# Kernel tuning notes

Hardware: AMD Instinct MI355X
Metric: run time of the kernel (lower is better)

The kernel has to match this reference:

```python
import jax, jax.numpy as jnp
import numpy as np

N = 262144   # tokens
L = 128      # ldims (per-direction LSTM feature size)
H = 128      # hidden_units
H2 = 128     # hidden2_units
R = 64       # number of relation labels


def setup_inputs() -> dict:
    key = jax.random.key(0)
    ks = jax.random.split(key, 12)
    glorot = lambda k, shape: jax.random.uniform(
        k, shape, jnp.float32, -1.0, 1.0) * np.sqrt(6.0 / (shape[0] + shape[1]))
    return {
        "fwd": jax.random.normal(ks[0], (N, L), jnp.float32),
        "bwd": jax.random.normal(ks[1], (N, L), jnp.float32),
        "gold_heads": jax.random.randint(ks[2], (N - 1,), 0, N),
        "gold_rels": jax.random.randint(ks[3], (N - 1,), 0, R),
        "WFOH": glorot(ks[4], (2 * L, H)),
        "WFOM": glorot(ks[5], (2 * L, H)),
        "rhidBias": glorot(ks[6], (1, H)),
        "rcatBias": glorot(ks[7], (1, 2 * H)),
        "rhid2Layer": glorot(ks[8], (2 * H, H2)),
        "rhid2Bias": glorot(ks[9], (1, H2)),
        "routLayer": glorot(ks[10], (H2, R)),
        "routBias": glorot(ks[11], (1, R)),
    }


def reference(fwd, bwd, gold_heads, gold_rels, WFOH, WFOM, rhidBias,
              rcatBias, rhid2Layer, rhid2Bias, routLayer, routBias):
    E = gold_heads.shape[0]
    mods = jnp.arange(E) + 1                       # modifiers are tokens 1..N-1
    # per-edge concat(head fwd-state, modifier bwd-state): (E, 2L)
    cat = jnp.concatenate([fwd[gold_heads], bwd[mods]], axis=-1)
    headfov = cat @ WFOH                           # (E, H)
    modfov = cat @ WFOM                            # (E, H)
    # hidden2_units > 0 branch of __evaluateLabel
    h = jnp.tanh(jnp.concatenate([headfov, modfov], axis=-1) + rcatBias)  # (E, 2H)
    h2 = jnp.tanh(h @ rhid2Layer + rhid2Bias)      # (E, H2)
    scores = h2 @ routLayer + routBias             # (E, R)
    # hinge: best wrong label vs gold label, loss only if margin violated
    gold_s = jnp.take_along_axis(scores, gold_rels[:, None], axis=1)[:, 0]
    masked = jnp.where(jnp.arange(R)[None, :] == gold_rels[:, None], -jnp.inf, scores)
    wrong_idx = jnp.argmax(masked, axis=1)
    wrong_s = jnp.take_along_axis(scores, wrong_idx[:, None], axis=1)[:, 0]
    lerrs = jnp.where(gold_s < wrong_s + 1.0, wrong_s - gold_s, 0.0)  # (E,)
    return lerrs
```

## Files before the change

kernel.cpp:

```cpp
#include <hip/hip_runtime.h>
#include <hip/hip_bf16.h>

typedef __bf16 bf16x8 __attribute__((ext_vector_type(8)));
typedef __bf16 bf16x2 __attribute__((ext_vector_type(2)));
typedef float  f32x4  __attribute__((ext_vector_type(4)));

#define MFMA16 __builtin_amdgcn_mfma_f32_16x16x32_bf16

__device__ __forceinline__ float fast_tanh(float x) {
    float e = __builtin_amdgcn_exp2f(x * 2.8853900817779268f);
    return 1.0f - 2.0f * __builtin_amdgcn_rcpf(e + 1.0f);
}

__device__ __forceinline__ int kinv(int ke) {
    return (ke & ~31) | ((ke & 1) << 4) | ((ke >> 1) & 15);
}

__global__ __launch_bounds__(256) void preconv_kernel(
    const float* __restrict__ WFOH, const float* __restrict__ WFOM,
    const float* __restrict__ rhid2Layer, const float* __restrict__ routLayer,
    char* __restrict__ ws)
{
    const int f = blockIdx.x * 256 + threadIdx.x;
    bf16x8 v;
    char* dst;
    if (f < 8192) {
        const int lane = f & 63, t = f >> 6;
        const int nbl = t & 1, kk = (t >> 1) & 7, w = t >> 4;
        const int g = lane >> 4, c = lane & 15;
        const int nb = 32 * w + 16 * nbl;
        const float* Wsrc = (nb < 128) ? WFOH : WFOM;
        const int col = (nb + c) & 127;
        #pragma unroll
        for (int j = 0; j < 8; ++j) v[j] = (__bf16)Wsrc[(32 * kk + 8 * g + j) * 128 + col];
        dst = ws + (size_t)f * 16;
    } else if (f < 12288) {
        const int f2 = f - 8192;
        const int lane = f2 & 63, t = f2 >> 6;
        const int nbl = t & 1, kk = (t >> 1) & 7, q4 = t >> 4;
        const int g = lane >> 4, c = lane & 15;
        const int n2 = 32 * q4 + 16 * nbl + c;
        #pragma unroll
        for (int j = 0; j < 8; ++j) v[j] = (__bf16)rhid2Layer[kinv(32 * kk + 8 * g + j) * 128 + n2];
        dst = ws + 131072 + (size_t)f2 * 16;
    } else if (f < 13312) {
        const int f3 = f - 12288;
        const int lane = f3 & 63, t = f3 >> 6;
        const int kk = t & 3, q4 = t >> 2;
        const int g = lane >> 4, c = lane & 15;
        const int n3 = 16 * q4 + c;
        #pragma unroll
        for (int j = 0; j < 8; ++j) v[j] = (__bf16)routLayer[kinv(32 * kk + 8 * g + j) * 64 + n3];
        dst = ws + 196608 + (size_t)f3 * 16;
    } else {
        return;
    }
    *(bf16x8*)dst = v;
}

template<bool PRE>
__device__ __forceinline__ bf16x8 wfrag1(const char* ws, const float* WFOH, const float* WFOM,
                                         int w, int kk, int nbl, int lane) {
    if constexpr (PRE) {
        return *(const bf16x8*)(ws + (size_t)w * 16384 + kk * 2048 + nbl * 1024 + lane * 16);
    } else {
        const int g = lane >> 4, c = lane & 15;
        const int nb = 32 * w + 16 * nbl;
        const float* Wsrc = (nb < 128) ? WFOH : WFOM;
        const int col = (nb + c) & 127;
        bf16x8 v;
        #pragma unroll
        for (int j = 0; j < 8; ++j) v[j] = (__bf16)Wsrc[(32 * kk + 8 * g + j) * 128 + col];
        return v;
    }
}
template<bool PRE>
__device__ __forceinline__ bf16x8 wfrag2(const char* ws, const float* rhid2Layer,
                                         int q4, int kk, int nbl, int lane) {
    if constexpr (PRE) {
        return *(const bf16x8*)(ws + 131072 + (size_t)q4 * 16384 + kk * 2048 + nbl * 1024 + lane * 16);
    } else {
        const int g = lane >> 4, c = lane & 15;
        const int n2 = 32 * q4 + 16 * nbl + c;
        bf16x8 v;
        #pragma unroll
        for (int j = 0; j < 8; ++j) v[j] = (__bf16)rhid2Layer[kinv(32 * kk + 8 * g + j) * 128 + n2];
        return v;
    }
}
template<bool PRE>
__device__ __forceinline__ bf16x8 wfrag3(const char* ws, const float* routLayer,
                                         int q4, int kk, int lane) {
    if constexpr (PRE) {
        return *(const bf16x8*)(ws + 196608 + (size_t)q4 * 4096 + kk * 1024 + lane * 16);
    } else {
        const int g = lane >> 4, c = lane & 15;
        const int n3 = 16 * q4 + c;
        bf16x8 v;
        #pragma unroll
        for (int j = 0; j < 8; ++j) v[j] = (__bf16)routLayer[kinv(32 * kk + 8 * g + j) * 64 + n3];
        return v;
    }
}

template<bool PRE>
__global__ __launch_bounds__(512, 2) void rel_kernel(
    const float* __restrict__ fwd, const float* __restrict__ bwd,
    const int* __restrict__ gold_heads, const int* __restrict__ gold_rels,
    const float* __restrict__ WFOH, const float* __restrict__ WFOM,
    const float* __restrict__ rcatBias, const float* __restrict__ rhid2Layer,
    const float* __restrict__ rhid2Bias, const float* __restrict__ routLayer,
    const float* __restrict__ routBias, const char* __restrict__ ws,
    float* __restrict__ out, int E, int NT)
{
    __shared__ __align__(16) char smem[131072];
    __shared__ int sh_nfix;
    __shared__ int sh_fixlist[16];

    char* const sh_cat = smem;
    char* const sh_h   = smem + 65536;
    float* const fx_cat = (float*)(smem + 98304);
    float* const fx_h   = fx_cat + 256;
    float* const fx_h2  = fx_h + 256;
    float* const fx_p   = fx_h2 + 128;

    const int tid   = threadIdx.x;
    const int w     = tid >> 6;
    const int lane  = tid & 63;
    const int row16 = lane & 15;
    const int g     = lane >> 4;
    const int xm    = (row16 & 7) << 4;
    const int q4    = w & 3;
    const int hw    = w >> 2;

    const int r_s = tid >> 2;
    const int q_s = tid & 3;
    const int xr  = (r_s & 7) << 4;

    const float rcb0 = rcatBias[32 * w + row16];
    const float rcb1 = rcatBias[32 * w + 16 + row16];
    const float r2b0 = rhid2Bias[32 * q4 + row16];
    const float r2b1 = rhid2Bias[32 * q4 + 16 + row16];
    const float rob  = routBias[16 * q4 + row16];

    bf16x8 pfb[8];
    {
        const int e = blockIdx.x * 128 + r_s;
        int nh = 0;
        if (q_s < 2 && e < E) nh = gold_heads[e];
        if (e < E) {
            const float* src = (q_s < 2) ? (fwd + (size_t)nh * 128 + 64 * q_s)
                                         : (bwd + (size_t)(e + 1) * 128 + 64 * (q_s - 2));
            const float4* p4 = (const float4*)src;
            #pragma unroll
            for (int i = 0; i < 8; ++i) {
                const float4 a = p4[2 * i], b = p4[2 * i + 1];
                bf16x8 t;
                t[0] = (__bf16)a.x; t[1] = (__bf16)a.y; t[2] = (__bf16)a.z; t[3] = (__bf16)a.w;
                t[4] = (__bf16)b.x; t[5] = (__bf16)b.y; t[6] = (__bf16)b.z; t[7] = (__bf16)b.w;
                pfb[i] = t;
            }
        } else {
            #pragma unroll
            for (int i = 0; i < 8; ++i) {
                bf16x8 t;
                #pragma unroll
                for (int j = 0; j < 8; ++j) t[j] = (__bf16)0.0f;
                pfb[i] = t;
            }
        }
    }

    for (int tile = blockIdx.x; tile < NT; tile += gridDim.x) {
        const int e0 = tile * 128;
        const int tnext = tile + gridDim.x;
        const bool hn = tnext < NT;

        #pragma unroll
        for (int i = 0; i < 8; ++i)
            *(bf16x8*)(sh_cat + r_s * 512 + ((128 * q_s + 16 * i) ^ xr)) = pfb[i];

        int nh = 0;
        bool gv = false;
        if (hn) {
            const int en = tnext * 128 + r_s;
            gv = en < E;
            if (q_s < 2 && gv) nh = gold_heads[en];
        }
        __syncthreads();

        f32x4 acc1[8][2];
        #pragma unroll
        for (int i = 0; i < 8; ++i) {
            acc1[i][0] = (f32x4){0.f, 0.f, 0.f, 0.f};
            acc1[i][1] = (f32x4){0.f, 0.f, 0.f, 0.f};
        }
        #pragma unroll 1
        for (int kk = 0; kk < 8; ++kk) {
            const bf16x8 b0 = wfrag1<PRE>(ws, WFOH, WFOM, w, kk, 0, lane);
            const bf16x8 b1 = wfrag1<PRE>(ws, WFOH, WFOM, w, kk, 1, lane);
            const int ko = (64 * kk + 16 * g) ^ xm;
            #pragma unroll
            for (int mb = 0; mb < 8; ++mb) {
                const bf16x8 a = *(const bf16x8*)(sh_cat + (16 * mb + row16) * 512 + ko);
                acc1[mb][0] = MFMA16(a, b0, acc1[mb][0], 0, 0, 0);
                acc1[mb][1] = MFMA16(a, b1, acc1[mb][1], 0, 0, 0);
            }
        }
        #pragma unroll
        for (int mb = 0; mb < 8; ++mb) {
            #pragma unroll
            for (int r = 0; r < 4; ++r) {
                const int row = 16 * mb + 4 * g + r;
                bf16x2 p;
                p[0] = (__bf16)fast_tanh(acc1[mb][0][r] + rcb0);
                p[1] = (__bf16)fast_tanh(acc1[mb][1][r] + rcb1);
                *(bf16x2*)(sh_h + row * 512 + ((64 * w + 4 * row16) ^ ((row & 7) << 4))) = p;
            }
        }
        __syncthreads();

        const float* gsrc = nullptr;
        if (hn) {
            const int en = tnext * 128 + r_s;
            gsrc = (q_s < 2) ? (fwd + (size_t)nh * 128 + 64 * q_s)
                             : (bwd + (size_t)(en + 1) * 128 + 64 * (q_s - 2));
        }
        float4 pfA[8];
        if (hn && gv) {
            const float4* p4 = (const float4*)gsrc;
            #pragma unroll
            for (int i = 0; i < 8; ++i) pfA[i] = p4[i];
        } else {
            #pragma unroll
            for (int i = 0; i < 8; ++i) pfA[i] = make_float4(0.f, 0.f, 0.f, 0.f);
        }

        f32x4 acc2[4][2];
        #pragma unroll
        for (int i = 0; i < 4; ++i) {
            acc2[i][0] = (f32x4){0.f, 0.f, 0.f, 0.f};
            acc2[i][1] = (f32x4){0.f, 0.f, 0.f, 0.f};
        }
        #pragma unroll 1
        for (int kk = 0; kk < 8; ++kk) {
            const bf16x8 b0 = wfrag2<PRE>(ws, rhid2Layer, q4, kk, 0, lane);
            const bf16x8 b1 = wfrag2<PRE>(ws, rhid2Layer, q4, kk, 1, lane);
            const int ko = (64 * kk + 16 * g) ^ xm;
            #pragma unroll
            for (int i = 0; i < 4; ++i) {
                const bf16x8 a = *(const bf16x8*)(sh_h + (16 * (4 * hw + i) + row16) * 512 + ko);
                acc2[i][0] = MFMA16(a, b0, acc2[i][0], 0, 0, 0);
                acc2[i][1] = MFMA16(a, b1, acc2[i][1], 0, 0, 0);
            }
        }
        #pragma unroll
        for (int i = 0; i < 4; ++i) {
            const float4 a = pfA[2 * i], b = pfA[2 * i + 1];
            bf16x8 t;
            t[0] = (__bf16)a.x; t[1] = (__bf16)a.y; t[2] = (__bf16)a.z; t[3] = (__bf16)a.w;
            t[4] = (__bf16)b.x; t[5] = (__bf16)b.y; t[6] = (__bf16)b.z; t[7] = (__bf16)b.w;
            pfb[i] = t;
        }
        float4 pfB[8];
        if (hn && gv) {
            const float4* p4 = (const float4*)gsrc;
            #pragma unroll
            for (int i = 0; i < 8; ++i) pfB[i] = p4[8 + i];
        } else {
            #pragma unroll
            for (int i = 0; i < 8; ++i) pfB[i] = make_float4(0.f, 0.f, 0.f, 0.f);
        }
        #pragma unroll
        for (int i = 0; i < 4; ++i) {
            #pragma unroll
            for (int r = 0; r < 4; ++r) {
                const int row = 16 * (4 * hw + i) + 4 * g + r;
                bf16x2 p;
                p[0] = (__bf16)fast_tanh(acc2[i][0][r] + r2b0);
                p[1] = (__bf16)fast_tanh(acc2[i][1][r] + r2b1);
                *(bf16x2*)(sh_cat + row * 256 + ((64 * q4 + 4 * row16) ^ ((row & 7) << 4))) = p;
            }
        }
        __syncthreads();

        if (tid == 0) sh_nfix = 0;
        f32x4 acc3[4];
        #pragma unroll
        for (int i = 0; i < 4; ++i) acc3[i] = (f32x4){0.f, 0.f, 0.f, 0.f};
        #pragma unroll
        for (int kk = 0; kk < 4; ++kk) {
            const bf16x8 b = wfrag3<PRE>(ws, routLayer, q4, kk, lane);
            const int ko = (64 * kk + 16 * g) ^ xm;
            #pragma unroll
            for (int i = 0; i < 4; ++i) {
                const bf16x8 a = *(const bf16x8*)(sh_cat + (16 * (4 * hw + i) + row16) * 256 + ko);
                acc3[i] = MFMA16(a, b, acc3[i], 0, 0, 0);
            }
        }
        #pragma unroll
        for (int i = 0; i < 4; ++i) {
            const float4 a = pfB[2 * i], b = pfB[2 * i + 1];
            bf16x8 t;
            t[0] = (__bf16)a.x; t[1] = (__bf16)a.y; t[2] = (__bf16)a.z; t[3] = (__bf16)a.w;
            t[4] = (__bf16)b.x; t[5] = (__bf16)b.y; t[6] = (__bf16)b.z; t[7] = (__bf16)b.w;
            pfb[4 + i] = t;
        }
        #pragma unroll
        for (int i = 0; i < 4; ++i) {
            #pragma unroll
            for (int r = 0; r < 4; ++r) {
                const int row = 16 * (4 * hw + i) + 4 * g + r;
                *(float*)(sh_h + row * 256 + ((64 * q4 + 4 * row16) ^ ((row & 7) << 4))) = acc3[i][r] + rob;
            }
        }
        __syncthreads();

        {
            const int r = tid >> 2, q = tid & 3;
            const int e = e0 + r;
            const int gold = (e < E) ? gold_rels[e] : 0;
            float gs = -3.0e38f, ws_ = -3.0e38f;
            #pragma unroll
            for (int c = 0; c < 4; ++c) {
                const f32x4 sv = *(const f32x4*)(sh_h + r * 256 + ((64 * q + 16 * c) ^ ((r & 7) << 4)));
                #pragma unroll
                for (int cc = 0; cc < 4; ++cc) {
                    const int lab = 16 * q + 4 * c + cc;
                    const float v = sv[cc];
                    if (lab == gold) gs = v; else ws_ = fmaxf(ws_, v);
                }
            }
            gs = fmaxf(gs, __shfl_xor(gs, 1)); ws_ = fmaxf(ws_, __shfl_xor(ws_, 1));
            gs = fmaxf(gs, __shfl_xor(gs, 2)); ws_ = fmaxf(ws_, __shfl_xor(ws_, 2));
            if (q == 0 && e < E) {
                out[e] = (gs < ws_ + 1.0f) ? (ws_ - gs) : 0.0f;
                if (fabsf((gs - ws_) - 1.0f) < 0.125f) {
                    const int idx = atomicAdd(&sh_nfix, 1);
                    if (idx < 16) sh_fixlist[idx] = r;
                }
            }
        }
        __syncthreads();

        int nf = sh_nfix; if (nf > 16) nf = 16;
        for (int fi = 0; fi < nf; ++fi) {
            const int e = e0 + sh_fixlist[fi];
            if (tid < 256) {
                const int head = gold_heads[e];
                fx_cat[tid] = (tid < 128) ? fwd[(size_t)head * 128 + tid]
                                          : bwd[(size_t)(e + 1) * 128 + (tid - 128)];
            }
            __syncthreads();
            {
                const int d = tid & 255, half = tid >> 8;
                const float* base = (d < 128) ? WFOH : WFOM;
                const int col = d & 127;
                float s = 0.f;
                #pragma unroll 8
                for (int k = 128 * half; k < 128 * half + 128; ++k) s += fx_cat[k] * base[k * 128 + col];
                fx_p[half * 256 + d] = s;
            }
            __syncthreads();
            if (tid < 256) fx_h[tid] = tanhf(fx_p[tid] + fx_p[256 + tid] + rcatBias[tid]);
            __syncthreads();
            {
                const int d2 = tid & 127, qq = tid >> 7;
                float s = 0.f;
                #pragma unroll 8
                for (int k = 64 * qq; k < 64 * qq + 64; ++k) s += fx_h[k] * rhid2Layer[k * 128 + d2];
                fx_p[qq * 128 + d2] = s;
            }
            __syncthreads();
            if (tid < 128) fx_h2[tid] = tanhf(fx_p[tid] + fx_p[128 + tid] + fx_p[256 + tid] + fx_p[384 + tid] + rhid2Bias[tid]);
            __syncthreads();
            if (tid < 64) {
                float s = 0.f;
                #pragma unroll 8
                for (int k = 0; k < 128; ++k) s += fx_h2[k] * routLayer[k * 64 + tid];
                const float v = s + routBias[tid];
                const int gold = gold_rels[e];
                float gs = (tid == gold) ? v : -3.0e38f;
                float wv = (tid == gold) ? -3.0e38f : v;
                #pragma unroll
                for (int o = 1; o < 64; o <<= 1) {
                    gs = fmaxf(gs, __shfl_xor(gs, o));
                    wv = fmaxf(wv, __shfl_xor(wv, o));
                }
                if (tid == 0) out[e] = (gs < wv + 1.0f) ? (wv - gs) : 0.0f;
            }
            __syncthreads();
        }
    }
}

extern "C" void kernel_launch(void* const* d_in, const int* in_sizes, int n_in,
                              void* d_out, int out_size, void* d_ws, size_t ws_size,
                              hipStream_t stream) {
    const float* fwd        = (const float*)d_in[0];
    const float* bwd        = (const float*)d_in[1];
    const int*   gold_heads = (const int*)d_in[2];
    const int*   gold_rels  = (const int*)d_in[3];
    const float* WFOH       = (const float*)d_in[4];
    const float* WFOM       = (const float*)d_in[5];
    const float* rcatBias   = (const float*)d_in[7];
    const float* rhid2      = (const float*)d_in[8];
    const float* rhid2Bias  = (const float*)d_in[9];
    const float* rout       = (const float*)d_in[10];
    const float* routBias   = (const float*)d_in[11];
    float* out = (float*)d_out;

    const int E = in_sizes[2];
    if (E <= 0) return;
    const int NT = (E + 127) / 128;
    const int grid = NT < 256 ? NT : 256;

    if (ws_size >= (size_t)212992) {
        hipLaunchKernelGGL(preconv_kernel, dim3(52), dim3(256), 0, stream,
                           WFOH, WFOM, rhid2, rout, (char*)d_ws);
        hipLaunchKernelGGL((rel_kernel<true>), dim3(grid), dim3(512), 0, stream,
                           fwd, bwd, gold_heads, gold_rels, WFOH, WFOM, rcatBias,
                           rhid2, rhid2Bias, rout, routBias, (const char*)d_ws, out, E, NT);
    } else {
        hipLaunchKernelGGL((rel_kernel<false>), dim3(grid), dim3(512), 0, stream,
                           fwd, bwd, gold_heads, gold_rels, WFOH, WFOM, rcatBias,
                           rhid2, rhid2Bias, rout, routBias, (const char*)nullptr, out, E, NT);
    }
}
```

Baseline: 157.4 us.

## Halve tile to 64 edges, shrink LDS and double blocks per CU

Shrinks each block's edge tile from 128 to 64 rows. Shared memory drops to 64KB by aliasing the h2 and score buffers onto the cat/h regions, and launch bounds allow 4 blocks of 512 threads per CU with a grid of 512. The warp work split is reorganised for each GEMM stage, and the weight fragment for the next k step is now loaded one iteration ahead in the first two GEMM loops. The aim is more resident waves to hide gather latency, at the cost of a tighter register budget and less weight reuse per tile.

```diff
diff --git a/kernel.cpp b/kernel.cpp
--- a/kernel.cpp
+++ b/kernel.cpp
@@ -2,7 +2,6 @@
 #include <hip/hip_bf16.h>
 
 typedef __bf16 bf16x8 __attribute__((ext_vector_type(8)));
-typedef __bf16 bf16x2 __attribute__((ext_vector_type(2)));
 typedef float  f32x4  __attribute__((ext_vector_type(4)));
 
 #define MFMA16 __builtin_amdgcn_mfma_f32_16x16x32_bf16
@@ -14,6 +13,13 @@
 
 __device__ __forceinline__ int kinv(int ke) {
     return (ke & ~31) | ((ke & 1) << 4) | ((ke >> 1) & 15);
+}
+
+__device__ __forceinline__ bf16x8 cvt2(const float4 a, const float4 b) {
+    bf16x8 t;
+    t[0] = (__bf16)a.x; t[1] = (__bf16)a.y; t[2] = (__bf16)a.z; t[3] = (__bf16)a.w;
+    t[4] = (__bf16)b.x; t[5] = (__bf16)b.y; t[6] = (__bf16)b.z; t[7] = (__bf16)b.w;
+    return t;
 }
 
 __global__ __launch_bounds__(256) void preconv_kernel(
@@ -104,7 +110,7 @@
 }
 
 template<bool PRE>
-__global__ __launch_bounds__(512, 2) void rel_kernel(
+__global__ __launch_bounds__(512, 4) void rel_kernel(
     const float* __restrict__ fwd, const float* __restrict__ bwd,
     const int* __restrict__ gold_heads, const int* __restrict__ gold_rels,
     const float* __restrict__ WFOH, const float* __restrict__ WFOM,
@@ -113,13 +119,15 @@
     const float* __restrict__ routBias, const char* __restrict__ ws,
     float* __restrict__ out, int E, int NT)
 {
-    __shared__ __align__(16) char smem[131072];
+    __shared__ __align__(16) char smem[65536];
     __shared__ int sh_nfix;
     __shared__ int sh_fixlist[16];
 
     char* const sh_cat = smem;
-    char* const sh_h   = smem + 65536;
-    float* const fx_cat = (float*)(smem + 98304);
+    char* const sh_h   = smem + 32768;
+    char* const sh_h2  = smem;
+    char* const sh_sc  = smem + 32768;
+    float* const fx_cat = (float*)(smem + 16384);
     float* const fx_h   = fx_cat + 256;
     float* const fx_h2  = fx_h + 256;
     float* const fx_p   = fx_h2 + 128;
@@ -130,209 +138,192 @@
     const int row16 = lane & 15;
     const int g     = lane >> 4;
     const int xm    = (row16 & 7) << 4;
-    const int q4    = w & 3;
-    const int hw    = w >> 2;
-
-    const int r_s = tid >> 2;
-    const int q_s = tid & 3;
+    const int mw    = w >> 2;
+    const int nw    = w & 3;
+
+    const int r_s = tid >> 3;
+    const int q_s = tid & 7;
     const int xr  = (r_s & 7) << 4;
 
     const float rcb0 = rcatBias[32 * w + row16];
     const float rcb1 = rcatBias[32 * w + 16 + row16];
-    const float r2b0 = rhid2Bias[32 * q4 + row16];
-    const float r2b1 = rhid2Bias[32 * q4 + 16 + row16];
-    const float rob  = routBias[16 * q4 + row16];
-
-    bf16x8 pfb[8];
+    const float r2b  = rhid2Bias[16 * w + row16];
+    const float rob  = routBias[16 * nw + row16];
+
+    bf16x8 pfb[4];
     {
-        const int e = blockIdx.x * 128 + r_s;
+        const int e = blockIdx.x * 64 + r_s;
         int nh = 0;
-        if (q_s < 2 && e < E) nh = gold_heads[e];
+        if (q_s < 4 && e < E) nh = gold_heads[e];
         if (e < E) {
-            const float* src = (q_s < 2) ? (fwd + (size_t)nh * 128 + 64 * q_s)
-                                         : (bwd + (size_t)(e + 1) * 128 + 64 * (q_s - 2));
+            const float* src = (q_s < 4) ? (fwd + (size_t)nh * 128 + 32 * q_s)
+                                         : (bwd + (size_t)(e + 1) * 128 + 32 * (q_s - 4));
             const float4* p4 = (const float4*)src;
             #pragma unroll
-            for (int i = 0; i < 8; ++i) {
-                const float4 a = p4[2 * i], b = p4[2 * i + 1];
-                bf16x8 t;
-                t[0] = (__bf16)a.x; t[1] = (__bf16)a.y; t[2] = (__bf16)a.z; t[3] = (__bf16)a.w;
-                t[4] = (__bf16)b.x; t[5] = (__bf16)b.y; t[6] = (__bf16)b.z; t[7] = (__bf16)b.w;
-                pfb[i] = t;
-            }
+            for (int i = 0; i < 4; ++i) pfb[i] = cvt2(p4[2 * i], p4[2 * i + 1]);
         } else {
             #pragma unroll
-            for (int i = 0; i < 8; ++i) {
-                bf16x8 t;
-                #pragma unroll
-                for (int j = 0; j < 8; ++j) t[j] = (__bf16)0.0f;
-                pfb[i] = t;
-            }
+            for (int i = 0; i < 4; ++i) pfb[i] = cvt2(make_float4(0.f,0.f,0.f,0.f), make_float4(0.f,0.f,0.f,0.f));
         }
     }
 
     for (int tile = blockIdx.x; tile < NT; tile += gridDim.x) {
-        const int e0 = tile * 128;
+        const int e0 = tile * 64;
         const int tnext = tile + gridDim.x;
         const bool hn = tnext < NT;
 
         #pragma unroll
-        for (int i = 0; i < 8; ++i)
-            *(bf16x8*)(sh_cat + r_s * 512 + ((128 * q_s + 16 * i) ^ xr)) = pfb[i];
+        for (int i = 0; i < 4; ++i)
+            *(bf16x8*)(sh_cat + r_s * 512 + ((64 * q_s + 16 * i) ^ xr)) = pfb[i];
 
         int nh = 0;
         bool gv = false;
         if (hn) {
-            const int en = tnext * 128 + r_s;
+            const int en = tnext * 64 + r_s;
             gv = en < E;
-            if (q_s < 2 && gv) nh = gold_heads[en];
+            if (q_s < 4 && gv) nh = gold_heads[en];
         }
         __syncthreads();
 
-        f32x4 acc1[8][2];
-        #pragma unroll
-        for (int i = 0; i < 8; ++i) {
+        f32x4 acc1[4][2];
+        #pragma unroll
+        for (int i = 0; i < 4; ++i) {
             acc1[i][0] = (f32x4){0.f, 0.f, 0.f, 0.f};
             acc1[i][1] = (f32x4){0.f, 0.f, 0.f, 0.f};
         }
-        #pragma unroll 1
-        for (int kk = 0; kk < 8; ++kk) {
-            const bf16x8 b0 = wfrag1<PRE>(ws, WFOH, WFOM, w, kk, 0, lane);
-            const bf16x8 b1 = wfrag1<PRE>(ws, WFOH, WFOM, w, kk, 1, lane);
-            const int ko = (64 * kk + 16 * g) ^ xm;
-            #pragma unroll
-            for (int mb = 0; mb < 8; ++mb) {
-                const bf16x8 a = *(const bf16x8*)(sh_cat + (16 * mb + row16) * 512 + ko);
-                acc1[mb][0] = MFMA16(a, b0, acc1[mb][0], 0, 0, 0);
-                acc1[mb][1] = MFMA16(a, b1, acc1[mb][1], 0, 0, 0);
-            }
-        }
-        #pragma unroll
-        for (int mb = 0; mb < 8; ++mb) {
+        {
+            bf16x8 b0 = wfrag1<PRE>(ws, WFOH, WFOM, w, 0, 0, lane);
+            bf16x8 b1 = wfrag1<PRE>(ws, WFOH, WFOM, w, 0, 1, lane);
+            #pragma unroll 1
+            for (int kk = 0; kk < 8; ++kk) {
+                const bf16x8 nb0 = wfrag1<PRE>(ws, WFOH, WFOM, w, (kk + 1) & 7, 0, lane);
+                const bf16x8 nb1 = wfrag1<PRE>(ws, WFOH, WFOM, w, (kk + 1) & 7, 1, lane);
+                const int ko = (64 * kk + 16 * g) ^ xm;
+                #pragma unroll
+                for (int mb = 0; mb < 4; ++mb) {
+                    const bf16x8 a = *(const bf16x8*)(sh_cat + (16 * mb + row16) * 512 + ko);
+                    acc1[mb][0] = MFMA16(a, b0, acc1[mb][0], 0, 0, 0);
+                    acc1[mb][1] = MFMA16(a, b1, acc1[mb][1], 0, 0, 0);
+                }
+                b0 = nb0; b1 = nb1;
+            }
+        }
+        #pragma unroll
+        for (int mb = 0; mb < 4; ++mb) {
             #pragma unroll
             for (int r = 0; r < 4; ++r) {
                 const int row = 16 * mb + 4 * g + r;
-                bf16x2 p;
-                p[0] = (__bf16)fast_tanh(acc1[mb][0][r] + rcb0);
-                p[1] = (__bf16)fast_tanh(acc1[mb][1][r] + rcb1);
-                *(bf16x2*)(sh_h + row * 512 + ((64 * w + 4 * row16) ^ ((row & 7) << 4))) = p;
+                __bf16 p0 = (__bf16)fast_tanh(acc1[mb][0][r] + rcb0);
+                __bf16 p1 = (__bf16)fast_tanh(acc1[mb][1][r] + rcb1);
+                unsigned short u0 = __builtin_bit_cast(unsigned short, p0);
+                unsigned short u1 = __builtin_bit_cast(unsigned short, p1);
+                *(unsigned*)(sh_h + row * 512 + ((64 * w + 4 * row16) ^ ((row & 7) << 4)))
+                    = (unsigned)u0 | ((unsigned)u1 << 16);
             }
         }
         __syncthreads();
 
         const float* gsrc = nullptr;
         if (hn) {
-            const int en = tnext * 128 + r_s;
-            gsrc = (q_s < 2) ? (fwd + (size_t)nh * 128 + 64 * q_s)
-                             : (bwd + (size_t)(en + 1) * 128 + 64 * (q_s - 2));
-        }
-        float4 pfA[8];
+            const int en = tnext * 64 + r_s;
+            gsrc = (q_s < 4) ? (fwd + (size_t)nh * 128 + 32 * q_s)
+                             : (bwd + (size_t)(en + 1) * 128 + 32 * (q_s - 4));
+        }
+        float4 pfA[4];
         if (hn && gv) {
             const float4* p4 = (const float4*)gsrc;
             #pragma unroll
-            for (int i = 0; i < 8; ++i) pfA[i] = p4[i];
+            for (int i = 0; i < 4; ++i) pfA[i] = p4[i];
         } else {
             #pragma unroll
-            for (int i = 0; i < 8; ++i) pfA[i] = make_float4(0.f, 0.f, 0.f, 0.f);
-        }
-
-        f32x4 acc2[4][2];
-        #pragma unroll
-        for (int i = 0; i < 4; ++i) {
-            acc2[i][0] = (f32x4){0.f, 0.f, 0.f, 0.f};
-            acc2[i][1] = (f32x4){0.f, 0.f, 0.f, 0.f};
-        }
-        #pragma unroll 1
-        for (int kk = 0; kk < 8; ++kk) {
-            const bf16x8 b0 = wfrag2<PRE>(ws, rhid2Layer, q4, kk, 0, lane);
-            const bf16x8 b1 = wfrag2<PRE>(ws, rhid2Layer, q4, kk, 1, lane);
-            const int ko = (64 * kk + 16 * g) ^ xm;
-            #pragma unroll
-            for (int i = 0; i < 4; ++i) {
-                const bf16x8 a = *(const bf16x8*)(sh_h + (16 * (4 * hw + i) + row16) * 512 + ko);
-                acc2[i][0] = MFMA16(a, b0, acc2[i][0], 0, 0, 0);
-                acc2[i][1] = MFMA16(a, b1, acc2[i][1], 0, 0, 0);
-            }
-        }
-        #pragma unroll
-        for (int i = 0; i < 4; ++i) {
-            const float4 a = pfA[2 * i], b = pfA[2 * i + 1];
-            bf16x8 t;
-            t[0] = (__bf16)a.x; t[1] = (__bf16)a.y; t[2] = (__bf16)a.z; t[3] = (__bf16)a.w;
-            t[4] = (__bf16)b.x; t[5] = (__bf16)b.y; t[6] = (__bf16)b.z; t[7] = (__bf16)b.w;
-            pfb[i] = t;
-        }
-        float4 pfB[8];
+            for (int i = 0; i < 4; ++i) pfA[i] = make_float4(0.f, 0.f, 0.f, 0.f);
+        }
+
+        f32x4 acc2[4];
+        #pragma unroll
+        for (int i = 0; i < 4; ++i) acc2[i] = (f32x4){0.f, 0.f, 0.f, 0.f};
+        {
+            bf16x8 b2 = wfrag2<PRE>(ws, rhid2Layer, w >> 1, 0, w & 1, lane);
+            #pragma unroll 1
+            for (int kk = 0; kk < 8; ++kk) {
+                const bf16x8 nb2 = wfrag2<PRE>(ws, rhid2Layer, w >> 1, (kk + 1) & 7, w & 1, lane);
+                const int ko = (64 * kk + 16 * g) ^ xm;
+                #pragma unroll
+                for (int mb = 0; mb < 4; ++mb) {
+                    const bf16x8 a = *(const bf16x8*)(sh_h + (16 * mb + row16) * 512 + ko);
+                    acc2[mb] = MFMA16(a, b2, acc2[mb], 0, 0, 0);
+                }
+                b2 = nb2;
+            }
+        }
+        pfb[0] = cvt2(pfA[0], pfA[1]);
+        pfb[1] = cvt2(pfA[2], pfA[3]);
+        float4 pfB[4];
         if (hn && gv) {
             const float4* p4 = (const float4*)gsrc;
             #pragma unroll
-            for (int i = 0; i < 8; ++i) pfB[i] = p4[8 + i];
+            for (int i = 0; i < 4; ++i) pfB[i] = p4[4 + i];
         } else {
             #pragma unroll
-            for (int i = 0; i < 8; ++i) pfB[i] = make_float4(0.f, 0.f, 0.f, 0.f);
-        }
-        #pragma unroll
-        for (int i = 0; i < 4; ++i) {
+            for (int i = 0; i < 4; ++i) pfB[i] = make_float4(0.f, 0.f, 0.f, 0.f);
+        }
+        #pragma unroll
+        for (int mb = 0; mb < 4; ++mb) {
             #pragma unroll
             for (int r = 0; r < 4; ++r) {
-                const int row = 16 * (4 * hw + i) + 4 * g + r;
-                bf16x2 p;
-                p[0] = (__bf16)fast_tanh(acc2[i][0][r] + r2b0);
-                p[1] = (__bf16)fast_tanh(acc2[i][1][r] + r2b1);
-                *(bf16x2*)(sh_cat + row * 256 + ((64 * q4 + 4 * row16) ^ ((row & 7) << 4))) = p;
+                const int row = 16 * mb + 4 * g + r;
+                __bf16 p = (__bf16)fast_tanh(acc2[mb][r] + r2b);
+                *(unsigned short*)(sh_h2 + row * 256 +
+                    ((64 * (w >> 1) + 4 * row16 + 2 * (w & 1)) ^ ((row & 7) << 4)))
+                    = __builtin_bit_cast(unsigned short, p);
             }
         }
         __syncthreads();
 
         if (tid == 0) sh_nfix = 0;
-        f32x4 acc3[4];
-        #pragma unroll
-        for (int i = 0; i < 4; ++i) acc3[i] = (f32x4){0.f, 0.f, 0.f, 0.f};
+        f32x4 acc3[2];
+        acc3[0] = (f32x4){0.f, 0.f, 0.f, 0.f};
+        acc3[1] = (f32x4){0.f, 0.f, 0.f, 0.f};
         #pragma unroll
         for (int kk = 0; kk < 4; ++kk) {
-            const bf16x8 b = wfrag3<PRE>(ws, routLayer, q4, kk, lane);
+            const bf16x8 b = wfrag3<PRE>(ws, routLayer, nw, kk, lane);
             const int ko = (64 * kk + 16 * g) ^ xm;
             #pragma unroll
-            for (int i = 0; i < 4; ++i) {
-                const bf16x8 a = *(const bf16x8*)(sh_cat + (16 * (4 * hw + i) + row16) * 256 + ko);
+            for (int i = 0; i < 2; ++i) {
+                const bf16x8 a = *(const bf16x8*)(sh_h2 + (32 * mw + 16 * i + row16) * 256 + ko);
                 acc3[i] = MFMA16(a, b, acc3[i], 0, 0, 0);
             }
         }
-        #pragma unroll
-        for (int i = 0; i < 4; ++i) {
-            const float4 a = pfB[2 * i], b = pfB[2 * i + 1];
-            bf16x8 t;
-            t[0] = (__bf16)a.x; t[1] = (__bf16)a.y; t[2] = (__bf16)a.z; t[3] = (__bf16)a.w;
-            t[4] = (__bf16)b.x; t[5] = (__bf16)b.y; t[6] = (__bf16)b.z; t[7] = (__bf16)b.w;
-            pfb[4 + i] = t;
-        }
-        #pragma unroll
-        for (int i = 0; i < 4; ++i) {
+        pfb[2] = cvt2(pfB[0], pfB[1]);
+        pfb[3] = cvt2(pfB[2], pfB[3]);
+        #pragma unroll
+        for (int i = 0; i < 2; ++i) {
             #pragma unroll
             for (int r = 0; r < 4; ++r) {
-                const int row = 16 * (4 * hw + i) + 4 * g + r;
-                *(float*)(sh_h + row * 256 + ((64 * q4 + 4 * row16) ^ ((row & 7) << 4))) = acc3[i][r] + rob;
+                const int row = 32 * mw + 16 * i + 4 * g + r;
+                const int col = 16 * nw + row16;
+                *(float*)(sh_sc + row * 256 + ((4 * col) ^ ((row & 7) << 4))) = acc3[i][r] + rob;
             }
         }
         __syncthreads();
 
         {
-            const int r = tid >> 2, q = tid & 3;
+            const int r = tid >> 3, q = tid & 7;
             const int e = e0 + r;
             const int gold = (e < E) ? gold_rels[e] : 0;
+            const int xrh = (r & 7) << 4;
+            const f32x4 s0 = *(const f32x4*)(sh_sc + r * 256 + ((32 * q) ^ xrh));
+            const f32x4 s1 = *(const f32x4*)(sh_sc + r * 256 + ((32 * q + 16) ^ xrh));
             float gs = -3.0e38f, ws_ = -3.0e38f;
             #pragma unroll
-            for (int c = 0; c < 4; ++c) {
-                const f32x4 sv = *(const f32x4*)(sh_h + r * 256 + ((64 * q + 16 * c) ^ ((r & 7) << 4)));
-                #pragma unroll
-                for (int cc = 0; cc < 4; ++cc) {
-                    const int lab = 16 * q + 4 * c + cc;
-                    const float v = sv[cc];
-                    if (lab == gold) gs = v; else ws_ = fmaxf(ws_, v);
-                }
+            for (int cc = 0; cc < 4; ++cc) {
+                const int lab0 = 8 * q + cc, lab1 = 8 * q + 4 + cc;
+                if (lab0 == gold) gs = s0[cc]; else ws_ = fmaxf(ws_, s0[cc]);
+                if (lab1 == gold) gs = s1[cc]; else ws_ = fmaxf(ws_, s1[cc]);
             }
             gs = fmaxf(gs, __shfl_xor(gs, 1)); ws_ = fmaxf(ws_, __shfl_xor(ws_, 1));
             gs = fmaxf(gs, __shfl_xor(gs, 2)); ws_ = fmaxf(ws_, __shfl_xor(ws_, 2));
+            gs = fmaxf(gs, __shfl_xor(gs, 4)); ws_ = fmaxf(ws_, __shfl_xor(ws_, 4));
             if (q == 0 && e < E) {
                 out[e] = (gs < ws_ + 1.0f) ? (ws_ - gs) : 0.0f;
                 if (fabsf((gs - ws_) - 1.0f) < 0.125f) {
@@ -412,8 +403,8 @@
 
     const int E = in_sizes[2];
     if (E <= 0) return;
-    const int NT = (E + 127) / 128;
-    const int grid = NT < 256 ? NT : 256;
+    const int NT = (E + 63) / 64;
+    const int grid = NT < 512 ? NT : 512;
 
     if (ws_size >= (size_t)212992) {
         hipLaunchKernelGGL(preconv_kernel, dim3(52), dim3(256), 0, stream,
```

Result: slower. 283.5 us (+80.2%).
